# Performance work log

Measured on AMD Instinct MI355X. Metric: run time of the kernel, lower is better.

## Reference

```python
import jax, jax.numpy as jnp
import numpy as np

EPS = 1e-8


def _corners(boxes):
    # boxes (...,7): x,y,z,dx,dy,dz,yaw -> BEV corners (...,4,2), CCW order
    x, y = boxes[..., 0], boxes[..., 1]
    hx, hy = boxes[..., 3] * 0.5, boxes[..., 4] * 0.5
    yaw = boxes[..., 6]
    c, s = jnp.cos(yaw), jnp.sin(yaw)
    lx = jnp.stack([hx, -hx, -hx, hx], -1)   # (...,4)
    ly = jnp.stack([hy, hy, -hy, -hy], -1)
    cx = x[..., None] + c[..., None] * lx - s[..., None] * ly
    cy = y[..., None] + s[..., None] * lx + c[..., None] * ly
    return jnp.stack([cx, cy], -1)


def _in_box(pts, box):
    # pts (K,2), box (7,): point-in-rotated-rect test (boundary inclusive)
    c, s = jnp.cos(box[6]), jnp.sin(box[6])
    d = pts - box[:2]
    lx = c * d[:, 0] + s * d[:, 1]
    ly = -s * d[:, 0] + c * d[:, 1]
    return (jnp.abs(lx) <= box[3] * 0.5 + 1e-6) & (jnp.abs(ly) <= box[4] * 0.5 + 1e-6)


def _pair_inter_area(ca, cb, boxa, boxb):
    # Intersection area of two convex quads ca, cb (4,2).
    # Candidates: 16 edge-edge intersections + corners of A in B + corners of B in A.
    a1, a2 = ca, jnp.roll(ca, -1, axis=0)
    b1, b2 = cb, jnp.roll(cb, -1, axis=0)
    da, db = a2 - a1, b2 - b1
    den = da[:, None, 0] * db[None, :, 1] - da[:, None, 1] * db[None, :, 0]  # (4,4)
    diff = b1[None, :, :] - a1[:, None, :]                                    # (4,4,2)
    den_s = jnp.where(jnp.abs(den) < EPS, 1.0, den)
    t = (diff[..., 0] * db[None, :, 1] - diff[..., 1] * db[None, :, 0]) / den_s
    u = (diff[..., 0] * da[:, None, 1] - diff[..., 1] * da[:, None, 0]) / den_s
    ok = (jnp.abs(den) >= EPS) & (t >= 0.0) & (t <= 1.0) & (u >= 0.0) & (u <= 1.0)
    ipts = a1[:, None, :] + t[..., None] * da[:, None, :]
    pts = jnp.concatenate([ipts.reshape(16, 2), ca, cb], axis=0)   # (24,2)
    mask = jnp.concatenate([ok.reshape(16), _in_box(ca, boxb), _in_box(cb, boxa)], axis=0)
    cnt = mask.sum()
    # collapse invalid candidates onto one valid vertex (duplicates don't change shoelace)
    p0 = pts[jnp.argmax(mask)]
    pts = jnp.where(mask[:, None], pts, p0)
    ctr = (pts * mask[:, None]).sum(0) / jnp.maximum(cnt, 1)
    ang = jnp.arctan2(pts[:, 1] - ctr[1], pts[:, 0] - ctr[0])
    sp = pts[jnp.argsort(ang)]
    sn = jnp.roll(sp, -1, axis=0)
    area = 0.5 * jnp.abs(jnp.sum(sp[:, 0] * sn[:, 1] - sp[:, 1] * sn[:, 0]))
    return jnp.where(cnt >= 3, area, 0.0)


def boxes_iou_bev(ba, bb):
    # ba (N,7), bb (M,7) -> rotated BEV IoU matrix (N,M)
    ca, cb = _corners(ba), _corners(bb)
    area_a = ba[:, 3] * ba[:, 4]
    area_b = bb[:, 3] * bb[:, 4]
    pair_rows = jax.vmap(
        lambda c1, b1: jax.vmap(lambda c2, b2: _pair_inter_area(c1, c2, b1, b2))(cb, bb)
    )
    inter = pair_rows(ca, ba)                                    # (N,M)
    union = jnp.maximum(area_a[:, None] + area_b[None, :] - inter, EPS)
    return inter / union


def setup_inputs() -> dict:
    key = jax.random.key(0)
    N, M = 2048, 512
    ks = jax.random.split(key, 4)

    def make_boxes(k, n):
        kk = jax.random.split(k, 4)
        xy = jax.random.uniform(kk[0], (n, 2), minval=-50.0, maxval=50.0)
        z = jax.random.uniform(kk[1], (n, 1), minval=-3.0, maxval=1.0)
        dims = jax.random.uniform(kk[2], (n, 3), minval=0.5, maxval=5.5)
        yaw = jax.random.uniform(kk[3], (n, 1), minval=-np.pi, maxval=np.pi)
        return jnp.concatenate([xy, z, dims, yaw], axis=1).astype(jnp.float32)

    box_pred = make_boxes(ks[0], N)
    box_gt = make_boxes(ks[1], M)
    iou_pred = jax.random.normal(ks[2], (N, 1), dtype=jnp.float32)
    return {"iou_pred": iou_pred, "box_pred": box_pred, "box_gt": box_gt,
            "num_total_pos": 2048}


def reference(iou_pred, box_pred, box_gt, num_total_pos):
    target = boxes_iou_bev(box_pred[:, :7], box_gt[:, :7])   # (N,M)
    target = jnp.max(target, axis=1)                          # (N,)
    target = jax.lax.stop_gradient(2.0 * target - 1.0)
    loss = jnp.sum(jnp.abs(jnp.squeeze(iou_pred) - target))
    return loss / (num_total_pos + 1e-4)
```

## Files before the change

kernel.cpp:

```cpp
#include <hip/hip_runtime.h>
#include <math.h>

#define BLOCK 256
#define PSTRIDE 19

struct __align__(8) V2 { float x, y; };

__device__ __forceinline__ void box_corners(float x, float y, float hx, float hy,
                                            float c, float s, V2* out) {
    const float cx = c * hx, sx = s * hx, cy = c * hy, sy = s * hy;
    out[0].x = x + cx - sy; out[0].y = y + sx + cy;
    out[1].x = x - cx - sy; out[1].y = y - sx + cy;
    out[2].x = x - cx + sy; out[2].y = y - sx - cy;
    out[3].x = x + cx + sy; out[3].y = y + sx - cy;
}

__device__ float quad_inter_area(V2* __restrict__ buf, const V2* A, const V2* B) {
    int pO = 0, qO = 9;
    #pragma unroll
    for (int i = 0; i < 4; ++i) buf[pO + i] = A[i];
    int n = 4;

    #pragma unroll
    for (int k = 0; k < 4; ++k) {
        const V2 c1 = B[k];
        const V2 c2 = B[(k + 1) & 3];
        const float ex = c2.x - c1.x, ey = c2.y - c1.y;
        int m = 0;
        V2 vp = buf[pO + n - 1];
        float dp = ex * (vp.y - c1.y) - ey * (vp.x - c1.x);
        for (int i = 0; i < n; ++i) {
            const V2 vc = buf[pO + i];
            const float dc = ex * (vc.y - c1.y) - ey * (vc.x - c1.x);
            const bool inc = (dc >= 0.f), inp = (dp >= 0.f);
            if (inc != inp) {
                const float t = dp / (dp - dc);
                V2 X; X.x = vp.x + t * (vc.x - vp.x); X.y = vp.y + t * (vc.y - vp.y);
                if (m < 9) buf[qO + m] = X;
                ++m;
            }
            if (inc) {
                if (m < 9) buf[qO + m] = vc;
                ++m;
            }
            vp = vc; dp = dc;
        }
        n = (m < 9) ? m : 9;
        if (n < 3) return 0.f;
        const int t_ = pO; pO = qO; qO = t_;
    }

    const V2 v0 = buf[pO];
    V2 vp = v0;
    float area = 0.f;
    for (int i = 1; i < n; ++i) {
        const V2 vc = buf[pO + i];
        area += vp.x * vc.y - vp.y * vc.x;
        vp = vc;
    }
    area += vp.x * v0.y - vp.y * v0.x;
    return 0.5f * fabsf(area);
}

__global__ __launch_bounds__(BLOCK) void iou_row_kernel(
    const float* __restrict__ iou_pred,
    const float* __restrict__ box_pred,
    const float* __restrict__ box_gt,
    float* __restrict__ rowloss,
    int M)
{
    __shared__ int s_n;
    __shared__ int s_idx[512];
    __shared__ float s_red[BLOCK];
    __shared__ V2  s_poly[64 * PSTRIDE];

    const int tid = threadIdx.x;
    const int i = blockIdx.x;
    if (tid == 0) s_n = 0;

    const float ax   = box_pred[i * 7 + 0];
    const float ay   = box_pred[i * 7 + 1];
    const float adx  = box_pred[i * 7 + 3];
    const float ady  = box_pred[i * 7 + 4];
    const float ayaw = box_pred[i * 7 + 6];
    const float ahx = 0.5f * adx, ahy = 0.5f * ady;
    const float area_a = adx * ady;
    const float ra = sqrtf(ahx * ahx + ahy * ahy);
    V2 CA[4];
    box_corners(ax, ay, ahx, ahy, cosf(ayaw), sinf(ayaw), CA);
    __syncthreads();

    for (int j = tid; j < M; j += BLOCK) {
        const float bx  = box_gt[j * 7 + 0];
        const float by  = box_gt[j * 7 + 1];
        const float bdx = box_gt[j * 7 + 3];
        const float bdy = box_gt[j * 7 + 4];
        const float rb = 0.5f * sqrtf(bdx * bdx + bdy * bdy);
        const float dx = bx - ax, dy = by - ay;
        const float rr = ra + rb;
        if (dx * dx + dy * dy <= rr * rr) {
            const int pos = atomicAdd(&s_n, 1);
            if (pos < 512) s_idx[pos] = j;
        }
    }
    __syncthreads();

    float mymax = 0.f;
    if (tid < 64) {
        V2* buf = &s_poly[tid * PSTRIDE];
        const int ns = (s_n < 512) ? s_n : 512;
        for (int k = tid; k < ns; k += 64) {
            const int j = s_idx[k];
            const float bx   = box_gt[j * 7 + 0];
            const float by   = box_gt[j * 7 + 1];
            const float bdx  = box_gt[j * 7 + 3];
            const float bdy  = box_gt[j * 7 + 4];
            const float byaw = box_gt[j * 7 + 6];
            V2 CB[4];
            box_corners(bx, by, 0.5f * bdx, 0.5f * bdy, cosf(byaw), sinf(byaw), CB);
            const float inter = quad_inter_area(buf, CA, CB);
            const float uni = fmaxf(area_a + bdx * bdy - inter, 1e-8f);
            mymax = fmaxf(mymax, inter / uni);
        }
    }

    s_red[tid] = mymax;
    __syncthreads();
    for (int s = BLOCK / 2; s > 0; s >>= 1) {
        if (tid < s) s_red[tid] = fmaxf(s_red[tid], s_red[tid + s]);
        __syncthreads();
    }
    if (tid == 0) {
        const float target = 2.f * s_red[0] - 1.f;
        rowloss[i] = fabsf(iou_pred[i] - target);
    }
}

__global__ __launch_bounds__(256) void loss_reduce_kernel(
    const float* __restrict__ rowloss,
    const int* __restrict__ ntp,
    float* __restrict__ out,
    int N)
{
    __shared__ float s[256];
    float acc = 0.f;
    for (int i = threadIdx.x; i < N; i += 256) acc += rowloss[i];
    s[threadIdx.x] = acc;
    __syncthreads();
    for (int k = 128; k > 0; k >>= 1) {
        if (threadIdx.x < k) s[threadIdx.x] += s[threadIdx.x + k];
        __syncthreads();
    }
    if (threadIdx.x == 0) out[0] = s[0] / ((float)ntp[0] + 1e-4f);
}

extern "C" void kernel_launch(void* const* d_in, const int* in_sizes, int n_in,
                              void* d_out, int out_size, void* d_ws, size_t ws_size,
                              hipStream_t stream) {
    const float* iou_pred = (const float*)d_in[0];
    const float* box_pred = (const float*)d_in[1];
    const float* box_gt   = (const float*)d_in[2];
    const int*   ntp      = (const int*)d_in[3];
    float* out     = (float*)d_out;
    float* rowloss = (float*)d_ws;

    const int N = in_sizes[0];
    const int M = in_sizes[2] / 7;

    iou_row_kernel<<<N, BLOCK, 0, stream>>>(iou_pred, box_pred, box_gt, rowloss, M);
    loss_reduce_kernel<<<1, 256, 0, stream>>>(rowloss, ntp, out, N);
}
```

Before: 16.18 us.

## Replace polygon clipping with edge-clipping area, single-wave blocks, fused final reduction

Computes the intersection area as a sum of per-edge clipped line integrals (Green's theorem) in registers instead of Sutherland-Hodgman clipping through a shared-memory buffer. Blocks shrink to one 64-lane wavefront, which uses ballot/popcount compaction for candidates and shuffle reductions for the row max. The separate loss-reduction kernel is replaced by a last-block-done atomic counter that needs a memset launch. Coordinates are made relative to the pred box, which should help precision. Edge cases such as collinear or degenerate edges may behave differently.

Measured after the change: 62.67 us. 3.87x slower.

```diff
diff --git a/kernel.cpp b/kernel.cpp
--- a/kernel.cpp
+++ b/kernel.cpp
@@ -1,8 +1,5 @@
 #include <hip/hip_runtime.h>
 #include <math.h>
-
-#define BLOCK 256
-#define PSTRIDE 19
 
 struct __align__(8) V2 { float x, y; };
 
@@ -15,68 +12,42 @@
     out[3].x = x + cx + sy; out[3].y = y + sx - cy;
 }
 
-__device__ float quad_inter_area(V2* __restrict__ buf, const V2* A, const V2* B) {
-    int pO = 0, qO = 9;
+__device__ __forceinline__ float clip_edges(const V2* E, const V2* C) {
+    float acc = 0.f;
     #pragma unroll
-    for (int i = 0; i < 4; ++i) buf[pO + i] = A[i];
-    int n = 4;
-
-    #pragma unroll
-    for (int k = 0; k < 4; ++k) {
-        const V2 c1 = B[k];
-        const V2 c2 = B[(k + 1) & 3];
-        const float ex = c2.x - c1.x, ey = c2.y - c1.y;
-        int m = 0;
-        V2 vp = buf[pO + n - 1];
-        float dp = ex * (vp.y - c1.y) - ey * (vp.x - c1.x);
-        for (int i = 0; i < n; ++i) {
-            const V2 vc = buf[pO + i];
-            const float dc = ex * (vc.y - c1.y) - ey * (vc.x - c1.x);
-            const bool inc = (dc >= 0.f), inp = (dp >= 0.f);
-            if (inc != inp) {
-                const float t = dp / (dp - dc);
-                V2 X; X.x = vp.x + t * (vc.x - vp.x); X.y = vp.y + t * (vc.y - vp.y);
-                if (m < 9) buf[qO + m] = X;
-                ++m;
-            }
-            if (inc) {
-                if (m < 9) buf[qO + m] = vc;
-                ++m;
-            }
-            vp = vc; dp = dc;
+    for (int e = 0; e < 4; ++e) {
+        const V2 P = E[e], Q = E[(e + 1) & 3];
+        const float dx = Q.x - P.x, dy = Q.y - P.y;
+        float t0 = 0.f, t1 = 1.f;
+        #pragma unroll
+        for (int k = 0; k < 4; ++k) {
+            const V2 c1 = C[k], c2 = C[(k + 1) & 3];
+            const float ex = c2.x - c1.x, ey = c2.y - c1.y;
+            const float a = ex * (P.y - c1.y) - ey * (P.x - c1.x);
+            const float b = ex * dy - ey * dx;
+            if (b > 1e-12f)        t0 = fmaxf(t0, -a / b);
+            else if (b < -1e-12f)  t1 = fminf(t1, -a / b);
+            else if (a < 0.f)      t1 = -2.f;
         }
-        n = (m < 9) ? m : 9;
-        if (n < 3) return 0.f;
-        const int t_ = pO; pO = qO; qO = t_;
+        const float w = fmaxf(t1 - t0, 0.f);
+        acc += w * (P.x * dy - P.y * dx);
     }
-
-    const V2 v0 = buf[pO];
-    V2 vp = v0;
-    float area = 0.f;
-    for (int i = 1; i < n; ++i) {
-        const V2 vc = buf[pO + i];
-        area += vp.x * vc.y - vp.y * vc.x;
-        vp = vc;
-    }
-    area += vp.x * v0.y - vp.y * v0.x;
-    return 0.5f * fabsf(area);
+    return acc;
 }
 
-__global__ __launch_bounds__(BLOCK) void iou_row_kernel(
+__global__ __launch_bounds__(64) void iou_loss_kernel(
     const float* __restrict__ iou_pred,
     const float* __restrict__ box_pred,
     const float* __restrict__ box_gt,
+    const int* __restrict__ ntp,
+    int* __restrict__ counter,
     float* __restrict__ rowloss,
-    int M)
+    float* __restrict__ out,
+    int M, int N)
 {
-    __shared__ int s_n;
     __shared__ int s_idx[512];
-    __shared__ float s_red[BLOCK];
-    __shared__ V2  s_poly[64 * PSTRIDE];
-
-    const int tid = threadIdx.x;
     const int i = blockIdx.x;
-    if (tid == 0) s_n = 0;
+    const int lane = threadIdx.x;
 
     const float ax   = box_pred[i * 7 + 0];
     const float ay   = box_pred[i * 7 + 1];
@@ -87,71 +58,69 @@
     const float area_a = adx * ady;
     const float ra = sqrtf(ahx * ahx + ahy * ahy);
     V2 CA[4];
-    box_corners(ax, ay, ahx, ahy, cosf(ayaw), sinf(ayaw), CA);
-    __syncthreads();
+    box_corners(0.f, 0.f, ahx, ahy, cosf(ayaw), sinf(ayaw), CA);
 
-    for (int j = tid; j < M; j += BLOCK) {
-        const float bx  = box_gt[j * 7 + 0];
-        const float by  = box_gt[j * 7 + 1];
-        const float bdx = box_gt[j * 7 + 3];
-        const float bdy = box_gt[j * 7 + 4];
-        const float rb = 0.5f * sqrtf(bdx * bdx + bdy * bdy);
-        const float dx = bx - ax, dy = by - ay;
-        const float rr = ra + rb;
-        if (dx * dx + dy * dy <= rr * rr) {
-            const int pos = atomicAdd(&s_n, 1);
-            if (pos < 512) s_idx[pos] = j;
+    int base = 0;
+    for (int j0 = 0; j0 < M; j0 += 64) {
+        const int j = j0 + lane;
+        bool pass = false;
+        if (j < M) {
+            const float bx  = box_gt[j * 7 + 0];
+            const float by  = box_gt[j * 7 + 1];
+            const float bdx = box_gt[j * 7 + 3];
+            const float bdy = box_gt[j * 7 + 4];
+            const float rb = 0.5f * sqrtf(bdx * bdx + bdy * bdy);
+            const float dx = bx - ax, dy = by - ay;
+            const float rr = ra + rb;
+            pass = (dx * dx + dy * dy) <= rr * rr;
         }
+        const unsigned long long m = __ballot(pass);
+        if (pass) {
+            const int pos = base + __popcll(m & ((1ull << lane) - 1ull));
+            s_idx[pos] = j;
+        }
+        base += __popcll(m);
     }
     __syncthreads();
 
     float mymax = 0.f;
-    if (tid < 64) {
-        V2* buf = &s_poly[tid * PSTRIDE];
-        const int ns = (s_n < 512) ? s_n : 512;
-        for (int k = tid; k < ns; k += 64) {
-            const int j = s_idx[k];
-            const float bx   = box_gt[j * 7 + 0];
-            const float by   = box_gt[j * 7 + 1];
-            const float bdx  = box_gt[j * 7 + 3];
-            const float bdy  = box_gt[j * 7 + 4];
-            const float byaw = box_gt[j * 7 + 6];
-            V2 CB[4];
-            box_corners(bx, by, 0.5f * bdx, 0.5f * bdy, cosf(byaw), sinf(byaw), CB);
-            const float inter = quad_inter_area(buf, CA, CB);
-            const float uni = fmaxf(area_a + bdx * bdy - inter, 1e-8f);
-            mymax = fmaxf(mymax, inter / uni);
-        }
+    for (int k = lane; k < base; k += 64) {
+        const int j = s_idx[k];
+        const float bx   = box_gt[j * 7 + 0] - ax;
+        const float by   = box_gt[j * 7 + 1] - ay;
+        const float bdx  = box_gt[j * 7 + 3];
+        const float bdy  = box_gt[j * 7 + 4];
+        const float byaw = box_gt[j * 7 + 6];
+        V2 CB[4];
+        box_corners(bx, by, 0.5f * bdx, 0.5f * bdy, cosf(byaw), sinf(byaw), CB);
+        const float s2 = clip_edges(CA, CB) + clip_edges(CB, CA);
+        const float inter = 0.5f * fmaxf(s2, 0.f);
+        const float uni = fmaxf(area_a + bdx * bdy - inter, 1e-8f);
+        mymax = fmaxf(mymax, inter / uni);
     }
 
-    s_red[tid] = mymax;
-    __syncthreads();
-    for (int s = BLOCK / 2; s > 0; s >>= 1) {
-        if (tid < s) s_red[tid] = fmaxf(s_red[tid], s_red[tid + s]);
-        __syncthreads();
+    #pragma unroll
+    for (int off = 32; off > 0; off >>= 1)
+        mymax = fmaxf(mymax, __shfl_xor(mymax, off, 64));
+
+    if (lane == 0) {
+        const float target = 2.f * mymax - 1.f;
+        rowloss[i] = fabsf(iou_pred[i] - target);
+        __threadfence();
     }
-    if (tid == 0) {
-        const float target = 2.f * s_red[0] - 1.f;
-        rowloss[i] = fabsf(iou_pred[i] - target);
+
+    int old = 0;
+    if (lane == 0) old = atomicAdd(counter, 1);
+    old = __shfl(old, 0, 64);
+    if (old == N - 1) {
+        __threadfence();
+        float acc = 0.f;
+        for (int k = lane; k < N; k += 64) acc += rowloss[k];
+        #pragma unroll
+        for (int off = 32; off > 0; off >>= 1)
+            acc += __shfl_xor(acc, off, 64);
+        if (lane == 0) out[0] = acc / ((float)ntp[0] + 1e-4f);
     }
-}
-
-__global__ __launch_bounds__(256) void loss_reduce_kernel(
-    const float* __restrict__ rowloss,
-    const int* __restrict__ ntp,
-    float* __restrict__ out,
-    int N)
-{
-    __shared__ float s[256];
-    float acc = 0.f;
-    for (int i = threadIdx.x; i < N; i += 256) acc += rowloss[i];
-    s[threadIdx.x] = acc;
-    __syncthreads();
-    for (int k = 128; k > 0; k >>= 1) {
-        if (threadIdx.x < k) s[threadIdx.x] += s[threadIdx.x + k];
-        __syncthreads();
-    }
-    if (threadIdx.x == 0) out[0] = s[0] / ((float)ntp[0] + 1e-4f);
 }
 
 extern "C" void kernel_launch(void* const* d_in, const int* in_sizes, int n_in,
@@ -161,12 +130,15 @@
     const float* box_pred = (const float*)d_in[1];
     const float* box_gt   = (const float*)d_in[2];
     const int*   ntp      = (const int*)d_in[3];
-    float* out     = (float*)d_out;
-    float* rowloss = (float*)d_ws;
+    float* out = (float*)d_out;
+
+    int*   counter = (int*)d_ws;
+    float* rowloss = (float*)((char*)d_ws + 256);
 
     const int N = in_sizes[0];
     const int M = in_sizes[2] / 7;
 
-    iou_row_kernel<<<N, BLOCK, 0, stream>>>(iou_pred, box_pred, box_gt, rowloss, M);
-    loss_reduce_kernel<<<1, 256, 0, stream>>>(rowloss, ntp, out, N);
+    hipMemsetAsync(counter, 0, sizeof(int), stream);
+    iou_loss_kernel<<<N, 64, 0, stream>>>(iou_pred, box_pred, box_gt, ntp,
+                                          counter, rowloss, out, M, N);
 }
```
